# Kernel optimization log

Measured on AMD Instinct MI355X. Metric: run time of the kernel, lower is better.

The kernel has to match this reference:

```python
import jax, jax.numpy as jnp
import numpy as np

ORDER = 8  # polynomial order; w has ORDER+1 coefficients


def setup_inputs() -> dict:
    key = jax.random.key(0)
    kx, kw = jax.random.split(key)
    x = jax.random.normal(kx, (512, 65536), dtype=jnp.float32)
    # coefficients, shape [order+1, 1] as in the TF layer ('random' init ~ N(0, 0.05))
    w = jax.random.normal(kw, (ORDER + 1, 1), dtype=jnp.float32) * 0.05
    return {"x": x, "w": w}


def reference(x, w):
    # Faithful math: out = sum_{i=0}^{order} w[i] * x**i, elementwise
    # (original builds [B, F, order+1] powers then matmuls with w; Horner's
    # method computes the identical polynomial without the large intermediate).
    c = w[:, 0]  # [order+1]
    order = c.shape[0] - 1
    out = jnp.full_like(x, c[order])
    for i in range(order - 1, -1, -1):  # small fixed loop over coefficients
        out = out * x + c[i]
    return out
```

## Files before the change

kernel.cpp:

```cpp
#include <hip/hip_runtime.h>


typedef float f32x4 __attribute__((ext_vector_type(4)));

#define VPT 4

__global__ __launch_bounds__(256, 8) void taylor_poly_kernel(
    const f32x4* __restrict__ x,
    const float* __restrict__ w,
    f32x4* __restrict__ out,
    int n4)
{
    const float c0 = w[0], c1 = w[1], c2 = w[2], c3 = w[3], c4 = w[4];
    const float c5 = w[5], c6 = w[6], c7 = w[7], c8 = w[8];

    const int base = blockIdx.x * (blockDim.x * VPT) + threadIdx.x;
    const bool full = (base + (VPT - 1) * blockDim.x) < n4;

    f32x4 v[VPT];

    if (full) {
#pragma unroll
        for (int k = 0; k < VPT; ++k)
            v[k] = __builtin_nontemporal_load(&x[base + k * blockDim.x]);
    } else {
#pragma unroll
        for (int k = 0; k < VPT; ++k) {
            int i = base + k * blockDim.x;
            if (i < n4) v[k] = __builtin_nontemporal_load(&x[i]);
        }
    }

#pragma unroll
    for (int k = 0; k < VPT; ++k) {
        f32x4 r;
#pragma unroll
        for (int e = 0; e < 4; ++e) {
            float xv = v[k][e];
            float acc = fmaf(c8, xv, c7);
            acc = fmaf(acc, xv, c6);
            acc = fmaf(acc, xv, c5);
            acc = fmaf(acc, xv, c4);
            acc = fmaf(acc, xv, c3);
            acc = fmaf(acc, xv, c2);
            acc = fmaf(acc, xv, c1);
            acc = fmaf(acc, xv, c0);
            r[e] = acc;
        }
        v[k] = r;
    }

    if (full) {
#pragma unroll
        for (int k = 0; k < VPT; ++k)
            __builtin_nontemporal_store(v[k], &out[base + k * blockDim.x]);
    } else {
#pragma unroll
        for (int k = 0; k < VPT; ++k) {
            int i = base + k * blockDim.x;
            if (i < n4) __builtin_nontemporal_store(v[k], &out[i]);
        }
    }
}

extern "C" void kernel_launch(void* const* d_in, const int* in_sizes, int n_in,
                              void* d_out, int out_size, void* d_ws, size_t ws_size,
                              hipStream_t stream) {
    const float* x = (const float*)d_in[0];
    const float* w = (const float*)d_in[1];
    float* out = (float*)d_out;

    int n = in_sizes[0];
    int n4 = n >> 2;

    const int block = 256;
    const int elems_per_block = block * VPT;
    int grid = (n4 + elems_per_block - 1) / elems_per_block;

    taylor_poly_kernel<<<grid, block, 0, stream>>>(
        (const f32x4*)x, w, (f32x4*)out, n4);
}
```

Measured before the change: 220.3 us.

## Grid-stride loop with register double-buffered prefetch of next tile

Each block now processes four tiles in a grid-stride loop, issuing the loads for the next tile before computing and storing the current one. This cuts the block count by four and overlaps memory latency with the FMA chain inside each thread. An exact-size flag selects an unguarded fast path when the problem divides evenly. The cost is higher register use from the double buffer, which may reduce occupancy, and less block-level parallelism for a kernel that is purely memory-bound.

```diff
diff --git a/kernel.cpp b/kernel.cpp
--- a/kernel.cpp
+++ b/kernel.cpp
@@ -3,62 +3,88 @@
 
 typedef float f32x4 __attribute__((ext_vector_type(4)));
 
-#define VPT 4
+#define VPT   4
+#define ITERS 4
 
 __global__ __launch_bounds__(256, 8) void taylor_poly_kernel(
     const f32x4* __restrict__ x,
     const float* __restrict__ w,
     f32x4* __restrict__ out,
-    int n4)
+    int n4,
+    int exact)
 {
     const float c0 = w[0], c1 = w[1], c2 = w[2], c3 = w[3], c4 = w[4];
     const float c5 = w[5], c6 = w[6], c7 = w[7], c8 = w[8];
 
-    const int base = blockIdx.x * (blockDim.x * VPT) + threadIdx.x;
-    const bool full = (base + (VPT - 1) * blockDim.x) < n4;
+    const int tile   = blockDim.x * VPT;
+    const int stride = gridDim.x * tile;
+    int base = blockIdx.x * tile + threadIdx.x;
 
-    f32x4 v[VPT];
+    if (exact) {
+        f32x4 cur[VPT], nxt[VPT];
 
-    if (full) {
 #pragma unroll
         for (int k = 0; k < VPT; ++k)
-            v[k] = __builtin_nontemporal_load(&x[base + k * blockDim.x]);
-    } else {
-#pragma unroll
-        for (int k = 0; k < VPT; ++k) {
-            int i = base + k * blockDim.x;
-            if (i < n4) v[k] = __builtin_nontemporal_load(&x[i]);
-        }
-    }
+            cur[k] = __builtin_nontemporal_load(&x[base + k * blockDim.x]);
 
 #pragma unroll
-    for (int k = 0; k < VPT; ++k) {
-        f32x4 r;
+        for (int it = 0; it < ITERS; ++it) {
+            const int nbase = base + stride;
+            if (it + 1 < ITERS) {
 #pragma unroll
-        for (int e = 0; e < 4; ++e) {
-            float xv = v[k][e];
-            float acc = fmaf(c8, xv, c7);
-            acc = fmaf(acc, xv, c6);
-            acc = fmaf(acc, xv, c5);
-            acc = fmaf(acc, xv, c4);
-            acc = fmaf(acc, xv, c3);
-            acc = fmaf(acc, xv, c2);
-            acc = fmaf(acc, xv, c1);
-            acc = fmaf(acc, xv, c0);
-            r[e] = acc;
+                for (int k = 0; k < VPT; ++k)
+                    nxt[k] = __builtin_nontemporal_load(&x[nbase + k * blockDim.x]);
+            }
+
+#pragma unroll
+            for (int k = 0; k < VPT; ++k) {
+                f32x4 r;
+#pragma unroll
+                for (int e = 0; e < 4; ++e) {
+                    float xv = cur[k][e];
+                    float acc = fmaf(c8, xv, c7);
+                    acc = fmaf(acc, xv, c6);
+                    acc = fmaf(acc, xv, c5);
+                    acc = fmaf(acc, xv, c4);
+                    acc = fmaf(acc, xv, c3);
+                    acc = fmaf(acc, xv, c2);
+                    acc = fmaf(acc, xv, c1);
+                    acc = fmaf(acc, xv, c0);
+                    r[e] = acc;
+                }
+                __builtin_nontemporal_store(r, &out[base + k * blockDim.x]);
+            }
+
+#pragma unroll
+            for (int k = 0; k < VPT; ++k)
+                cur[k] = nxt[k];
+            base = nbase;
         }
-        v[k] = r;
-    }
-
-    if (full) {
+    } else {
+        for (int it = 0; it < ITERS; ++it) {
 #pragma unroll
-        for (int k = 0; k < VPT; ++k)
-            __builtin_nontemporal_store(v[k], &out[base + k * blockDim.x]);
-    } else {
+            for (int k = 0; k < VPT; ++k) {
+                int i = base + k * blockDim.x;
+                if (i < n4) {
+                    f32x4 v = __builtin_nontemporal_load(&x[i]);
+                    f32x4 r;
 #pragma unroll
-        for (int k = 0; k < VPT; ++k) {
-            int i = base + k * blockDim.x;
-            if (i < n4) __builtin_nontemporal_store(v[k], &out[i]);
+                    for (int e = 0; e < 4; ++e) {
+                        float xv = v[e];
+                        float acc = fmaf(c8, xv, c7);
+                        acc = fmaf(acc, xv, c6);
+                        acc = fmaf(acc, xv, c5);
+                        acc = fmaf(acc, xv, c4);
+                        acc = fmaf(acc, xv, c3);
+                        acc = fmaf(acc, xv, c2);
+                        acc = fmaf(acc, xv, c1);
+                        acc = fmaf(acc, xv, c0);
+                        r[e] = acc;
+                    }
+                    __builtin_nontemporal_store(r, &out[i]);
+                }
+            }
+            base += stride;
         }
     }
 }
@@ -74,9 +100,10 @@
     int n4 = n >> 2;
 
     const int block = 256;
-    const int elems_per_block = block * VPT;
-    int grid = (n4 + elems_per_block - 1) / elems_per_block;
+    const int per_block = block * VPT * ITERS;
+    int grid = (n4 + per_block - 1) / per_block;
+    int exact = (grid * per_block == n4) ? 1 : 0;
 
     taylor_poly_kernel<<<grid, block, 0, stream>>>(
-        (const f32x4*)x, w, (f32x4*)out, n4);
+        (const f32x4*)x, w, (f32x4*)out, n4, exact);
 }
```

Measured after the change: 219.7 us. About the same (-0.3%).
